# Optimization experiments

Hardware: AMD Instinct MI355X
Metric: run time of the kernel (lower is better)

## Reference

```python
import jax, jax.numpy as jnp
import numpy as np

DIM = 1024
HEADS = 16

def setup_inputs() -> dict:
    key = jax.random.key(0)
    k1, k2 = jax.random.split(key)
    x = jax.random.normal(k1, (4, 2048, DIM), dtype=jnp.float32)
    # torch nn.Linear(dim, 3*dim, bias=False): weight shape [3*dim, dim], y = x @ W.T
    W_qkv = jax.random.normal(k2, (3 * DIM, DIM), dtype=jnp.float32) * (DIM ** -0.5)
    return {"x": x, "W_qkv": W_qkv}

def reference(x, W_qkv):
    B, N, D = x.shape
    H = HEADS
    hd = D // H
    scale = hd ** -0.5
    qkv = jnp.einsum('bnd,ed->bne', x, W_qkv)            # [B,N,3D]
    qkv = qkv.reshape(B, N, 3, H, hd).transpose(2, 0, 3, 1, 4)  # [3,B,H,N,hd]
    q, k, v = qkv[0], qkv[1], qkv[2]
    attn = jnp.einsum('bhnd,bhmd->bhnm', q, k) * scale   # [B,H,N,N]
    attn = jax.nn.softmax(attn, axis=-1)                 # dropout is identity at eval
    out = jnp.einsum('bhnm,bhmd->bhnd', attn, v)         # [B,H,N,hd]
    return out.transpose(0, 2, 1, 3).reshape(B, N, D)
```

## Files before the change

kernel.cpp:

```cpp
#include <hip/hip_runtime.h>

typedef unsigned short ushort_t;
typedef short bf16x8 __attribute__((ext_vector_type(8)));
typedef float f32x4 __attribute__((ext_vector_type(4)));
typedef float f32x16 __attribute__((ext_vector_type(16)));

__device__ __forceinline__ unsigned f2bf(float f) {
  union { float f; unsigned u; } v; v.f = f;
  return (v.u + 0x7FFFu + ((v.u >> 16) & 1u)) >> 16;
}

__device__ __forceinline__ void gll16(const void* g, const void* l) {
  __builtin_amdgcn_global_load_lds(
      (const __attribute__((address_space(1))) void*)g,
      (__attribute__((address_space(3))) void*)l, 16, 0, 0);
}

__global__ __launch_bounds__(256) void cvt_bf16(const float* __restrict__ src,
                                                ushort_t* __restrict__ dst, int n4) {
  int i = blockIdx.x * 256 + threadIdx.x;
  if (i >= n4) return;
  float4 v = ((const float4*)src)[i];
  uint2 o;
  o.x = f2bf(v.x) | (f2bf(v.y) << 16);
  o.y = f2bf(v.z) | (f2bf(v.w) << 16);
  ((uint2*)dst)[i] = o;
}

__global__ __launch_bounds__(256) void gemm_qkv(const ushort_t* __restrict__ A,
                                                const ushort_t* __restrict__ Bw,
                                                ushort_t* __restrict__ C) {
  __shared__ ushort_t As[128 * 64];
  __shared__ ushort_t Bs[128 * 64];
  const int tid = threadIdx.x;
  const int w = tid >> 6, ln = tid & 63;
  const int g = ln >> 4, lr = ln & 15;
  const int bx = blockIdx.x;
  const int swz = (bx & 7) * 192 + (bx >> 3);
  const int nt = swz % 24, mt = swz / 24;
  const int m0 = mt * 128, n0 = nt * 128;
  const int wr = w >> 1, wc = w & 1;
  const float cscale = (nt < 8) ? 0.18033688f : 1.0f;

  f32x4 acc[4][4] = {};

  for (int kt = 0; kt < 16; ++kt) {
#pragma unroll
    for (int q = 0; q < 4; ++q) {
      int chunk = w * 256 + q * 64 + ln;
      int r = chunk >> 3, c = chunk & 7;
      int cs = c ^ (r & 7);
      gll16(A + (size_t)(m0 + r) * 1024 + kt * 64 + cs * 8, As + chunk * 8);
      gll16(Bw + (size_t)(n0 + r) * 1024 + kt * 64 + cs * 8, Bs + chunk * 8);
    }
    __syncthreads();
#pragma unroll
    for (int ks = 0; ks < 2; ++ks) {
      bf16x8 af[4], bfr[4];
#pragma unroll
      for (int mi = 0; mi < 4; ++mi) {
        int row = wr * 64 + mi * 16 + lr;
        af[mi] = *(const bf16x8*)((const char*)As + row * 128 +
                                  ((g * 16 + ks * 64) ^ ((row & 7) << 4)));
      }
#pragma unroll
      for (int ni = 0; ni < 4; ++ni) {
        int row = wc * 64 + ni * 16 + lr;
        bfr[ni] = *(const bf16x8*)((const char*)Bs + row * 128 +
                                   ((g * 16 + ks * 64) ^ ((row & 7) << 4)));
      }
#pragma unroll
      for (int mi = 0; mi < 4; ++mi)
#pragma unroll
        for (int ni = 0; ni < 4; ++ni)
          acc[mi][ni] = __builtin_amdgcn_mfma_f32_16x16x32_bf16(af[mi], bfr[ni],
                                                                acc[mi][ni], 0, 0, 0);
    }
    __syncthreads();
  }

#pragma unroll
  for (int mi = 0; mi < 4; ++mi)
#pragma unroll
    for (int ni = 0; ni < 4; ++ni)
#pragma unroll
      for (int r = 0; r < 4; ++r) {
        int row = m0 + wr * 64 + mi * 16 + g * 4 + r;
        int col = n0 + wc * 64 + ni * 16 + lr;
        C[(size_t)row * 3072 + col] = (ushort_t)f2bf(acc[mi][ni][r] * cscale);
      }
}

__global__ __launch_bounds__(256) void vtrans(const ushort_t* __restrict__ qkv,
                                              ushort_t* __restrict__ VT) {
  __shared__ ushort_t tl[64][72];
  int blk = blockIdx.x;
  int bh = blk >> 5, nb = blk & 31;
  int b = bh >> 4, h = bh & 15;
  int t = threadIdx.x;
  int r = t >> 2, c = t & 3;
  const ushort_t* src = qkv + (size_t)(b * 2048 + nb * 64 + r) * 3072 + 2048 + h * 64 + c * 16;
  uint2 v0 = *(const uint2*)(src);
  uint2 v1 = *(const uint2*)(src + 4);
  uint2 v2 = *(const uint2*)(src + 8);
  uint2 v3 = *(const uint2*)(src + 12);
  *(uint2*)&tl[r][c * 16] = v0;
  *(uint2*)&tl[r][c * 16 + 4] = v1;
  *(uint2*)&tl[r][c * 16 + 8] = v2;
  *(uint2*)&tl[r][c * 16 + 12] = v3;
  __syncthreads();
  int d = t >> 2, dc = t & 3;
  unsigned pk[8];
#pragma unroll
  for (int j = 0; j < 8; ++j) {
    unsigned lo = tl[dc * 16 + 2 * j][d];
    unsigned hi = tl[dc * 16 + 2 * j + 1][d];
    pk[j] = lo | (hi << 16);
  }
  ushort_t* dst = VT + (size_t)(bh * 64 + d) * 2048 + nb * 64 + dc * 16;
  uint4 o0; o0.x = pk[0]; o0.y = pk[1]; o0.z = pk[4]; o0.w = pk[5];
  uint4 o1; o1.x = pk[2]; o1.y = pk[3]; o1.z = pk[6]; o1.w = pk[7];
  *(uint4*)dst = o0;
  *(uint4*)(dst + 8) = o1;
}

__global__ __launch_bounds__(512) void attn2(const ushort_t* __restrict__ qkv,
                                             const ushort_t* __restrict__ VT,
                                             float* __restrict__ out) {
  __shared__ ushort_t Ks[3][2048];
  __shared__ ushort_t Vs[3][2048];
  const int blk = blockIdx.x;
  const int bh = blk & 63, qt = blk >> 6;
  const int b = bh >> 4, hh = bh & 15;
  const int tid = threadIdx.x;
  const int w = tid >> 6, l = tid & 63;
  const int q = l & 31, h = l >> 5;
  const int q0 = qt * 256 + w * 32;
  const int qsw = q & 7;

  const ushort_t* qrow = qkv + (size_t)(b * 2048 + q0 + q) * 3072 + hh * 64 + 8 * h;
  bf16x8 qf[4];
#pragma unroll
  for (int m = 0; m < 4; ++m) qf[m] = *(const bf16x8*)(qrow + 16 * m);

  const int st = tid & 255;
  const int rS = st >> 3, cS = st & 7;
  const int cL = cS ^ (rS & 7);
  const bool isK = tid < 256;
  const ushort_t* gsrc =
      isK ? qkv + (size_t)(b * 2048 + rS) * 3072 + 1024 + hh * 64 + cL * 8
          : VT + (size_t)(bh * 64 + rS + 32 * (cL >> 2)) * 2048 + (cL & 3) * 8;
  const size_t gstep = isK ? (size_t)32 * 3072 : (size_t)32;
  ushort_t* lbase = isK ? &Ks[0][0] : &Vs[0][0];

  f32x16 oacc0, oacc1;
#pragma unroll
  for (int i = 0; i < 16; ++i) { oacc0[i] = 0.f; oacc1[i] = 0.f; }
  float l_run = 0.f;

  gll16(gsrc, lbase + st * 8);
  gll16(gsrc + gstep, lbase + 2048 + st * 8);
  asm volatile("s_waitcnt vmcnt(1)" ::: "memory");
  __builtin_amdgcn_s_barrier();

  int cur = 0;
  for (int t = 0; t < 64; ++t) {
    int tn = t + 2; if (tn > 63) tn = 63;
    int bufn = cur + 2; if (bufn >= 3) bufn -= 3;
    gll16(gsrc + (size_t)tn * gstep, lbase + bufn * 2048 + st * 8);

    const ushort_t* KsB = Ks[cur];
    const ushort_t* VsB = Vs[cur];

    f32x16 S;
#pragma unroll
    for (int i = 0; i < 16; ++i) S[i] = 0.f;
    __builtin_amdgcn_s_setprio(1);
#pragma unroll
    for (int m = 0; m < 4; ++m) {
      bf16x8 kf = *(const bf16x8*)(KsB + q * 64 + (((2 * m + h) ^ qsw) * 8));
      S = __builtin_amdgcn_mfma_f32_32x32x16_bf16(kf, qf[m], S, 0, 0, 0);
    }
    __builtin_amdgcn_s_setprio(0);

    float p[16];
#pragma unroll
    for (int i = 0; i < 16; ++i) p[i] = __builtin_amdgcn_exp2f(S[i]);
    float s0 = (p[0] + p[1]) + (p[2] + p[3]);
    float s1 = (p[4] + p[5]) + (p[6] + p[7]);
    float s2 = (p[8] + p[9]) + (p[10] + p[11]);
    float s3 = (p[12] + p[13]) + (p[14] + p[15]);
    float ls = (s0 + s1) + (s2 + s3);
    ls += __shfl_xor(ls, 32, 64);
    l_run += ls;

    union { unsigned u[4]; bf16x8 v; } pf0, pf1;
#pragma unroll
    for (int i = 0; i < 4; ++i)
      asm("v_cvt_pk_bf16_f32 %0, %1, %2"
          : "=v"(pf0.u[i]) : "v"(p[2 * i]), "v"(p[2 * i + 1]));
#pragma unroll
    for (int i = 0; i < 4; ++i)
      asm("v_cvt_pk_bf16_f32 %0, %1, %2"
          : "=v"(pf1.u[i]) : "v"(p[8 + 2 * i]), "v"(p[8 + 2 * i + 1]));

    bf16x8 vf0 = *(const bf16x8*)(VsB + q * 64 + (((0 + h) ^ qsw) * 8));
    bf16x8 vf1 = *(const bf16x8*)(VsB + q * 64 + (((2 + h) ^ qsw) * 8));
    bf16x8 vf2 = *(const bf16x8*)(VsB + q * 64 + (((4 + h) ^ qsw) * 8));
    bf16x8 vf3 = *(const bf16x8*)(VsB + q * 64 + (((6 + h) ^ qsw) * 8));

    __builtin_amdgcn_s_setprio(1);
    oacc0 = __builtin_amdgcn_mfma_f32_32x32x16_bf16(vf0, pf0.v, oacc0, 0, 0, 0);
    oacc0 = __builtin_amdgcn_mfma_f32_32x32x16_bf16(vf1, pf1.v, oacc0, 0, 0, 0);
    oacc1 = __builtin_amdgcn_mfma_f32_32x32x16_bf16(vf2, pf0.v, oacc1, 0, 0, 0);
    oacc1 = __builtin_amdgcn_mfma_f32_32x32x16_bf16(vf3, pf1.v, oacc1, 0, 0, 0);
    __builtin_amdgcn_s_setprio(0);

    asm volatile("s_waitcnt vmcnt(1)" ::: "memory");
    __builtin_amdgcn_s_barrier();
    cur += 1; if (cur == 3) cur = 0;
  }

  float inv = 1.0f / l_run;
  float* orow = out + (size_t)(b * 2048 + q0 + q) * 1024 + hh * 64 + 4 * h;
#pragma unroll
  for (int rq = 0; rq < 4; ++rq) {
    float4 o0, o1;
    o0.x = oacc0[rq * 4 + 0] * inv; o0.y = oacc0[rq * 4 + 1] * inv;
    o0.z = oacc0[rq * 4 + 2] * inv; o0.w = oacc0[rq * 4 + 3] * inv;
    o1.x = oacc1[rq * 4 + 0] * inv; o1.y = oacc1[rq * 4 + 1] * inv;
    o1.z = oacc1[rq * 4 + 2] * inv; o1.w = oacc1[rq * 4 + 3] * inv;
    *(float4*)(orow + 8 * rq) = o0;
    *(float4*)(orow + 32 + 8 * rq) = o1;
  }
}

extern "C" void kernel_launch(void* const* d_in, const int* in_sizes, int n_in,
                              void* d_out, int out_size, void* d_ws, size_t ws_size,
                              hipStream_t stream) {
  const float* x = (const float*)d_in[0];
  const float* Wq = (const float*)d_in[1];
  float* out = (float*)d_out;
  char* ws = (char*)d_ws;

  ushort_t* xb = (ushort_t*)ws;
  ushort_t* wb = (ushort_t*)(ws + 16777216);
  ushort_t* qkv = (ushort_t*)(ws + 23068672);
  ushort_t* VT = xb;

  cvt_bf16<<<8192, 256, 0, stream>>>(x, xb, 8192 * 1024 / 4);
  cvt_bf16<<<3072, 256, 0, stream>>>(Wq, wb, 3072 * 1024 / 4);
  gemm_qkv<<<64 * 24, 256, 0, stream>>>(xb, wb, qkv);
  vtrans<<<64 * 32, 256, 0, stream>>>(qkv, VT);
  attn2<<<64 * 8, 512, 0, stream>>>(qkv, VT, out);
}
```

Measured before the change: 168.8 us.

## Fuse V transpose into QKV GEMM epilogue and split score accumulators

The GEMM epilogue now writes Q/K into a compact 2048-wide buffer and writes V directly in transposed per-head layout, which removes the separate vtrans kernel and its read/write round trip. In attention, the QK^T MFMA chain is split into two independent accumulators so consecutive MFMAs do not wait on each other, and the PV MFMAs are interleaved for the same reason. The per-iteration cross-lane row-sum shuffle is deferred to a single shuffle after the loop. The trade-offs are scattered 8-byte VT stores from the GEMM, one extra add per score element, and more workspace memory.

```diff
diff --git a/kernel.cpp b/kernel.cpp
--- a/kernel.cpp
+++ b/kernel.cpp
@@ -29,7 +29,8 @@
 
 __global__ __launch_bounds__(256) void gemm_qkv(const ushort_t* __restrict__ A,
                                                 const ushort_t* __restrict__ Bw,
-                                                ushort_t* __restrict__ C) {
+                                                ushort_t* __restrict__ qk,
+                                                ushort_t* __restrict__ VT) {
   __shared__ ushort_t As[128 * 64];
   __shared__ ushort_t Bs[128 * 64];
   const int tid = threadIdx.x;
@@ -79,52 +80,37 @@
     __syncthreads();
   }
 
-#pragma unroll
-  for (int mi = 0; mi < 4; ++mi)
-#pragma unroll
-    for (int ni = 0; ni < 4; ++ni)
-#pragma unroll
-      for (int r = 0; r < 4; ++r) {
-        int row = m0 + wr * 64 + mi * 16 + g * 4 + r;
-        int col = n0 + wc * 64 + ni * 16 + lr;
-        C[(size_t)row * 3072 + col] = (ushort_t)f2bf(acc[mi][ni][r] * cscale);
+  if (nt < 16) {
+#pragma unroll
+    for (int mi = 0; mi < 4; ++mi)
+#pragma unroll
+      for (int ni = 0; ni < 4; ++ni)
+#pragma unroll
+        for (int r = 0; r < 4; ++r) {
+          int row = m0 + wr * 64 + mi * 16 + g * 4 + r;
+          int col = n0 + wc * 64 + ni * 16 + lr;
+          qk[(size_t)row * 2048 + col] = (ushort_t)f2bf(acc[mi][ni][r] * cscale);
+        }
+  } else {
+    const int b = m0 >> 11;
+    const int gp = ((g & 1) << 1) | (g >> 1);
+#pragma unroll
+    for (int mi = 0; mi < 4; ++mi) {
+      int nbase = (m0 & 2047) + wr * 64 + mi * 16 + gp * 4;
+#pragma unroll
+      for (int ni = 0; ni < 4; ++ni) {
+        int f = n0 - 2048 + wc * 64 + ni * 16 + lr;
+        int hh = f >> 6, d = f & 63;
+        uint2 o;
+        o.x = f2bf(acc[mi][ni][0]) | (f2bf(acc[mi][ni][1]) << 16);
+        o.y = f2bf(acc[mi][ni][2]) | (f2bf(acc[mi][ni][3]) << 16);
+        *(uint2*)(VT + ((size_t)(b * 16 + hh) * 64 + d) * 2048 + nbase) = o;
       }
-}
-
-__global__ __launch_bounds__(256) void vtrans(const ushort_t* __restrict__ qkv,
-                                              ushort_t* __restrict__ VT) {
-  __shared__ ushort_t tl[64][72];
-  int blk = blockIdx.x;
-  int bh = blk >> 5, nb = blk & 31;
-  int b = bh >> 4, h = bh & 15;
-  int t = threadIdx.x;
-  int r = t >> 2, c = t & 3;
-  const ushort_t* src = qkv + (size_t)(b * 2048 + nb * 64 + r) * 3072 + 2048 + h * 64 + c * 16;
-  uint2 v0 = *(const uint2*)(src);
-  uint2 v1 = *(const uint2*)(src + 4);
-  uint2 v2 = *(const uint2*)(src + 8);
-  uint2 v3 = *(const uint2*)(src + 12);
-  *(uint2*)&tl[r][c * 16] = v0;
-  *(uint2*)&tl[r][c * 16 + 4] = v1;
-  *(uint2*)&tl[r][c * 16 + 8] = v2;
-  *(uint2*)&tl[r][c * 16 + 12] = v3;
-  __syncthreads();
-  int d = t >> 2, dc = t & 3;
-  unsigned pk[8];
-#pragma unroll
-  for (int j = 0; j < 8; ++j) {
-    unsigned lo = tl[dc * 16 + 2 * j][d];
-    unsigned hi = tl[dc * 16 + 2 * j + 1][d];
-    pk[j] = lo | (hi << 16);
-  }
-  ushort_t* dst = VT + (size_t)(bh * 64 + d) * 2048 + nb * 64 + dc * 16;
-  uint4 o0; o0.x = pk[0]; o0.y = pk[1]; o0.z = pk[4]; o0.w = pk[5];
-  uint4 o1; o1.x = pk[2]; o1.y = pk[3]; o1.z = pk[6]; o1.w = pk[7];
-  *(uint4*)dst = o0;
-  *(uint4*)(dst + 8) = o1;
-}
-
-__global__ __launch_bounds__(512) void attn2(const ushort_t* __restrict__ qkv,
+    }
+  }
+}
+
+__global__ __launch_bounds__(512) void attn2(const ushort_t* __restrict__ qk,
                                              const ushort_t* __restrict__ VT,
                                              float* __restrict__ out) {
   __shared__ ushort_t Ks[3][2048];
@@ -138,7 +124,7 @@
   const int q0 = qt * 256 + w * 32;
   const int qsw = q & 7;
 
-  const ushort_t* qrow = qkv + (size_t)(b * 2048 + q0 + q) * 3072 + hh * 64 + 8 * h;
+  const ushort_t* qrow = qk + (size_t)(b * 2048 + q0 + q) * 2048 + hh * 64 + 8 * h;
   bf16x8 qf[4];
 #pragma unroll
   for (int m = 0; m < 4; ++m) qf[m] = *(const bf16x8*)(qrow + 16 * m);
@@ -148,9 +134,9 @@
   const int cL = cS ^ (rS & 7);
   const bool isK = tid < 256;
   const ushort_t* gsrc =
-      isK ? qkv + (size_t)(b * 2048 + rS) * 3072 + 1024 + hh * 64 + cL * 8
+      isK ? qk + (size_t)(b * 2048 + rS) * 2048 + 1024 + hh * 64 + cL * 8
           : VT + (size_t)(bh * 64 + rS + 32 * (cL >> 2)) * 2048 + (cL & 3) * 8;
-  const size_t gstep = isK ? (size_t)32 * 3072 : (size_t)32;
+  const size_t gstep = isK ? (size_t)32 * 2048 : (size_t)32;
   ushort_t* lbase = isK ? &Ks[0][0] : &Vs[0][0];
 
   f32x16 oacc0, oacc1;
@@ -172,27 +158,30 @@
     const ushort_t* KsB = Ks[cur];
     const ushort_t* VsB = Vs[cur];
 
-    f32x16 S;
-#pragma unroll
-    for (int i = 0; i < 16; ++i) S[i] = 0.f;
+    f32x16 Sa, Sb;
+#pragma unroll
+    for (int i = 0; i < 16; ++i) { Sa[i] = 0.f; Sb[i] = 0.f; }
     __builtin_amdgcn_s_setprio(1);
-#pragma unroll
-    for (int m = 0; m < 4; ++m) {
-      bf16x8 kf = *(const bf16x8*)(KsB + q * 64 + (((2 * m + h) ^ qsw) * 8));
-      S = __builtin_amdgcn_mfma_f32_32x32x16_bf16(kf, qf[m], S, 0, 0, 0);
+    {
+      bf16x8 kf0 = *(const bf16x8*)(KsB + q * 64 + (((0 + h) ^ qsw) * 8));
+      bf16x8 kf1 = *(const bf16x8*)(KsB + q * 64 + (((2 + h) ^ qsw) * 8));
+      bf16x8 kf2 = *(const bf16x8*)(KsB + q * 64 + (((4 + h) ^ qsw) * 8));
+      bf16x8 kf3 = *(const bf16x8*)(KsB + q * 64 + (((6 + h) ^ qsw) * 8));
+      Sa = __builtin_amdgcn_mfma_f32_32x32x16_bf16(kf0, qf[0], Sa, 0, 0, 0);
+      Sb = __builtin_amdgcn_mfma_f32_32x32x16_bf16(kf2, qf[2], Sb, 0, 0, 0);
+      Sa = __builtin_amdgcn_mfma_f32_32x32x16_bf16(kf1, qf[1], Sa, 0, 0, 0);
+      Sb = __builtin_amdgcn_mfma_f32_32x32x16_bf16(kf3, qf[3], Sb, 0, 0, 0);
     }
     __builtin_amdgcn_s_setprio(0);
 
     float p[16];
 #pragma unroll
-    for (int i = 0; i < 16; ++i) p[i] = __builtin_amdgcn_exp2f(S[i]);
+    for (int i = 0; i < 16; ++i) p[i] = __builtin_amdgcn_exp2f(Sa[i] + Sb[i]);
     float s0 = (p[0] + p[1]) + (p[2] + p[3]);
     float s1 = (p[4] + p[5]) + (p[6] + p[7]);
     float s2 = (p[8] + p[9]) + (p[10] + p[11]);
     float s3 = (p[12] + p[13]) + (p[14] + p[15]);
-    float ls = (s0 + s1) + (s2 + s3);
-    ls += __shfl_xor(ls, 32, 64);
-    l_run += ls;
+    l_run += (s0 + s1) + (s2 + s3);
 
     union { unsigned u[4]; bf16x8 v; } pf0, pf1;
 #pragma unroll
@@ -211,8 +200,8 @@
 
     __builtin_amdgcn_s_setprio(1);
     oacc0 = __builtin_amdgcn_mfma_f32_32x32x16_bf16(vf0, pf0.v, oacc0, 0, 0, 0);
+    oacc1 = __builtin_amdgcn_mfma_f32_32x32x16_bf16(vf2, pf0.v, oacc1, 0, 0, 0);
     oacc0 = __builtin_amdgcn_mfma_f32_32x32x16_bf16(vf1, pf1.v, oacc0, 0, 0, 0);
-    oacc1 = __builtin_amdgcn_mfma_f32_32x32x16_bf16(vf2, pf0.v, oacc1, 0, 0, 0);
     oacc1 = __builtin_amdgcn_mfma_f32_32x32x16_bf16(vf3, pf1.v, oacc1, 0, 0, 0);
     __builtin_amdgcn_s_setprio(0);
 
@@ -221,6 +210,7 @@
     cur += 1; if (cur == 3) cur = 0;
   }
 
+  l_run += __shfl_xor(l_run, 32, 64);
   float inv = 1.0f / l_run;
   float* orow = out + (size_t)(b * 2048 + q0 + q) * 1024 + hh * 64 + 4 * h;
 #pragma unroll
@@ -245,12 +235,11 @@
 
   ushort_t* xb = (ushort_t*)ws;
   ushort_t* wb = (ushort_t*)(ws + 16777216);
-  ushort_t* qkv = (ushort_t*)(ws + 23068672);
-  ushort_t* VT = xb;
+  ushort_t* qk = (ushort_t*)(ws + 23068672);
+  ushort_t* VT = (ushort_t*)(ws + 23068672 + 33554432);
 
   cvt_bf16<<<8192, 256, 0, stream>>>(x, xb, 8192 * 1024 / 4);
   cvt_bf16<<<3072, 256, 0, stream>>>(Wq, wb, 3072 * 1024 / 4);
-  gemm_qkv<<<64 * 24, 256, 0, stream>>>(xb, wb, qkv);
-  vtrans<<<64 * 32, 256, 0, stream>>>(qkv, VT);
-  attn2<<<64 * 8, 512, 0, stream>>>(qkv, VT, out);
-}
+  gemm_qkv<<<64 * 24, 256, 0, stream>>>(xb, wb, qk, VT);
+  attn2<<<64 * 8, 512, 0, stream>>>(qk, VT, out);
+}
```

Measured after the change: 168.0 us. About the same (-0.5%).
